# Kernel tuning notes

Measured on AMD Instinct MI355X. Metric: run time of the kernel, lower is better.

Reference implementation:

```python
import jax, jax.numpy as jnp
import numpy as np

NEG_SLOPE = 0.2  # PyG GATConv default


def gat_layer(x, W, att_src, att_dst, bias, src, dst, concat):
    # x: [N, F_in]; W: [F_in, H*C]; att_src/att_dst: [H, C]; bias: [H*C] or [C]
    N = x.shape[0]
    H, C = att_src.shape
    h = (x @ W).reshape(N, H, C)                       # [N, H, C]
    a_s = jnp.einsum('nhc,hc->nh', h, att_src)         # [N, H]
    a_d = jnp.einsum('nhc,hc->nh', h, att_dst)
    e = jax.nn.leaky_relu(a_s[src] + a_d[dst], NEG_SLOPE)  # [E, H]
    # segment softmax over incoming edges of each destination node
    m = jax.ops.segment_max(e, dst, num_segments=N)
    m = jnp.where(jnp.isfinite(m), m, 0.0)
    ee = jnp.exp(e - m[dst])
    s = jax.ops.segment_sum(ee, dst, num_segments=N)
    alpha = ee / (s[dst] + 1e-16)                      # [E, H]
    out = jax.ops.segment_sum(h[src] * alpha[:, :, None], dst, num_segments=N)  # [N, H, C]
    out = out.reshape(N, H * C) if concat else out.mean(axis=1)
    return out + bias


def setup_inputs() -> dict:
    key = jax.random.key(0)
    ks = jax.random.split(key, 16)
    N, E, F_IN, NC = 100000, 3200000, 256, 40
    H, C = 8, 8  # hidden GATConv: heads=8, out=8 -> width 64
    inp = {}
    inp['features'] = jax.random.normal(ks[0], (N, F_IN), dtype=jnp.float32)
    inp['edge_index'] = jax.random.randint(ks[1], (2, E), 0, N, dtype=jnp.int64)
    def p(k, shape):
        return jax.random.normal(k, shape, dtype=jnp.float32) * 0.1
    # layer 0: in 256 -> 8 heads x 8 (concat -> 64)
    inp['W0'] = p(ks[2], (F_IN, H * C)); inp['as0'] = p(ks[3], (H, C)); inp['ad0'] = p(ks[4], (H, C)); inp['b0'] = jnp.zeros((H * C,), jnp.float32)
    # layer 1: 64 -> 8 heads x 8 (concat -> 64)
    inp['W1'] = p(ks[5], (H * C, H * C)); inp['as1'] = p(ks[6], (H, C)); inp['ad1'] = p(ks[7], (H, C)); inp['b1'] = jnp.zeros((H * C,), jnp.float32)
    # layer 2: 64 -> 1 head x n_classes (mean/no-concat)
    inp['W2'] = p(ks[8], (H * C, NC)); inp['as2'] = p(ks[9], (1, NC)); inp['ad2'] = p(ks[10], (1, NC)); inp['b2'] = jnp.zeros((NC,), jnp.float32)
    return inp


def reference(features, edge_index, W0, as0, ad0, b0, W1, as1, ad1, b1, W2, as2, ad2, b2):
    N = features.shape[0]
    loops = jnp.arange(N, dtype=edge_index.dtype)  # PyG GATConv adds self-loops by default
    src = jnp.concatenate([edge_index[0], loops])
    dst = jnp.concatenate([edge_index[1], loops])
    x = gat_layer(features, W0, as0, ad0, b0, src, dst, True)
    x = gat_layer(x, W1, as1, ad1, b1, src, dst, True)
    x = gat_layer(x, W2, as2, ad2, b2, src, dst, False)
    return jax.nn.log_softmax(x, axis=-1)
```

## Files before the change

kernel.cpp:

```cpp
#include <hip/hip_runtime.h>
#include <hip/hip_bf16.h>

#define NEG_SLOPE 0.2f
#define LOG2E 1.44269504f
#define EPB 8192
#define MAXBUCK 400
#define CAP 9216

typedef __attribute__((ext_vector_type(8))) short short8;
typedef __attribute__((ext_vector_type(4))) float f32x4;

__device__ __forceinline__ unsigned short f2bf(float x) {
    unsigned u = __float_as_uint(x);
    unsigned r = (u + 0x7FFFu + ((u >> 16) & 1u)) >> 16;
    return (unsigned short)r;
}

__device__ __forceinline__ float fexp2(float x) {
    return __builtin_amdgcn_exp2f(x);
}


__global__ __launch_bounds__(256) void binit_k(int* __restrict__ bcurE,
                                               int nbuck) {
    int b = blockIdx.x * 256 + threadIdx.x;
    if (b < nbuck) bcurE[b] = b * CAP;
}

__global__ __launch_bounds__(512) void bscatter_k(
    const int* __restrict__ srcs, const int* __restrict__ dsts,
    int* __restrict__ bcurE, int* __restrict__ pairs, int E, int nbuck) {
    __shared__ int lh[MAXBUCK];
    __shared__ int lbase[MAXBUCK];
    int t = threadIdx.x;
    if (t < nbuck) lh[t] = 0;
    __syncthreads();
    int base = blockIdx.x * EPB;
    int cnt = E - base;
    if (cnt > EPB) cnt = EPB;
    int nq = cnt >> 2;
    const int4* d4p = (const int4*)(dsts + base);
    const int4* s4p = (const int4*)(srcs + base);
    for (int i = t; i < nq; i += 512) {
        int4 d = d4p[i];
        atomicAdd(&lh[d.x >> 8], 1);
        atomicAdd(&lh[d.y >> 8], 1);
        atomicAdd(&lh[d.z >> 8], 1);
        atomicAdd(&lh[d.w >> 8], 1);
    }
    for (int i = (nq << 2) + t; i < cnt; i += 512)
        atomicAdd(&lh[dsts[base + i] >> 8], 1);
    __syncthreads();
    if (t < nbuck) {
        int c = lh[t];
        lbase[t] = c ? atomicAdd(&bcurE[t], c) : 0;
        lh[t] = 0;
    }
    __syncthreads();
    for (int i = t; i < nq; i += 512) {
        int4 d = d4p[i];
        int4 s = s4p[i];
        int b0 = d.x >> 8, b1 = d.y >> 8, b2 = d.z >> 8, b3 = d.w >> 8;
        int r0 = atomicAdd(&lh[b0], 1);
        int r1 = atomicAdd(&lh[b1], 1);
        int r2 = atomicAdd(&lh[b2], 1);
        int r3 = atomicAdd(&lh[b3], 1);
        pairs[lbase[b0] + r0] = (s.x << 8) | (d.x & 255);
        pairs[lbase[b1] + r1] = (s.y << 8) | (d.y & 255);
        pairs[lbase[b2] + r2] = (s.z << 8) | (d.z & 255);
        pairs[lbase[b3] + r3] = (s.w << 8) | (d.w & 255);
    }
    for (int i = (nq << 2) + t; i < cnt; i += 512) {
        int s = srcs[base + i], d = dsts[base + i];
        int r = atomicAdd(&lh[d >> 8], 1);
        pairs[lbase[d >> 8] + r] = (s << 8) | (d & 255);
    }
}

__global__ __launch_bounds__(512) void bscan_k(
    const int* __restrict__ bcurE, int* __restrict__ bstart, int nbuck) {
    __shared__ int csum[512];
    int t = threadIdx.x;
    int v = (t < nbuck) ? bcurE[t] - t * CAP : 0;
    csum[t] = v;
    __syncthreads();
    for (int off = 1; off < 512; off <<= 1) {
        int x = (t >= off) ? csum[t - off] : 0;
        __syncthreads();
        csum[t] += x;
        __syncthreads();
    }
    if (t < nbuck) bstart[t] = csum[t] - v;
}

__global__ __launch_bounds__(512) void bucket_sort_k(
    const int* __restrict__ pairs, const int* __restrict__ bcurE,
    const int* __restrict__ bstart, int* __restrict__ row_ptr,
    int* __restrict__ csr_src, int N, int Etot) {
    __shared__ int lh[256];
    __shared__ int sc[256];
    int b = blockIdx.x;
    int n0 = b << 8;
    int t = threadIdx.x;
    if (t < 256) lh[t] = 0;
    __syncthreads();
    int e0c = b * CAP, e1c = bcurE[b];
    for (int e = e0c + t; e < e1c; e += 512)
        atomicAdd(&lh[pairs[e] & 255], 1);
    __syncthreads();
    if (t < 256) sc[t] = lh[t];
    __syncthreads();
    for (int off = 1; off < 256; off <<= 1) {
        int x = (t < 256 && t >= off) ? sc[t - off] : 0;
        __syncthreads();
        if (t < 256) sc[t] += x;
        __syncthreads();
    }
    int e0g = bstart[b];
    if (t < 256) {
        int cntv = lh[t];
        int excl = sc[t] - cntv;
        int n = n0 + t;
        int rp = e0g + n0 + t + excl;
        if (n < N) {
            row_ptr[n] = rp;
            csr_src[rp] = n << 7;
        }
        lh[t] = rp + 1;
    }
    __syncthreads();
    for (int e = e0c + t; e < e1c; e += 512) {
        int p = pairs[e];
        int pos = atomicAdd(&lh[p & 255], 1);
        csr_src[pos] = (p >> 8) << 7;
    }
    if (b == 0 && t == 0) row_ptr[N] = Etot;
}


template <int K>
__global__ __launch_bounds__(256) void gemm_pack8_k(
    const float* __restrict__ x, const float* __restrict__ W,
    const float* __restrict__ a_src, const float* __restrict__ a_dst,
    char* __restrict__ hrec, float* __restrict__ asb,
    float* __restrict__ adb, int N) {
    constexpr int NT = 4;
    constexpr int KT = K / 32;
    constexpr size_t WF_BYTES = (size_t)KT * NT * 64 * 8 * sizeof(short);
    constexpr size_t H_BYTES = (size_t)64 * 65 * sizeof(float);
    __shared__ alignas(16) char smem[WF_BYTES > H_BYTES ? WF_BYTES : H_BYTES];
    short* Wf = (short*)smem;
    float* hL = (float*)smem;
    int tid = threadIdx.x;
    for (int f = tid; f < KT * NT * 64; f += 256) {
        int lane = f & 63;
        int ntk = f >> 6;
        int nt = ntk % NT, kt = ntk / NT;
        int q = lane >> 4, c = lane & 15;
        int n = nt * 16 + c;
        int k0 = kt * 32 + q * 8;
        short8 frag;
        #pragma unroll
        for (int j = 0; j < 8; ++j)
            frag[j] = (short)f2bf(W[(size_t)(k0 + j) * 64 + n]);
        *(short8*)&Wf[f * 8] = frag;
    }
    __syncthreads();
    int wave = tid >> 6, lane = tid & 63;
    int q = lane >> 4, c = lane & 15;
    int m0 = blockIdx.x * 64 + wave * 16;
    int arow = m0 + c;
    int arl = arow < N ? arow : N - 1;
    f32x4 acc[NT] = {};
    for (int kt = 0; kt < KT; ++kt) {
        const float* xp = x + (size_t)arl * K + kt * 32 + q * 8;
        float4 a0 = *(const float4*)xp;
        float4 a1 = *(const float4*)(xp + 4);
        float av[8] = {a0.x, a0.y, a0.z, a0.w, a1.x, a1.y, a1.z, a1.w};
        short8 af;
        #pragma unroll
        for (int j = 0; j < 8; ++j) af[j] = (short)f2bf(av[j]);
        #pragma unroll
        for (int nt = 0; nt < NT; ++nt) {
            short8 bf = *(const short8*)&Wf[((kt * NT + nt) * 64 + lane) * 8];
            acc[nt] = __builtin_amdgcn_mfma_f32_16x16x32_bf16(af, bf, acc[nt],
                                                              0, 0, 0);
        }
    }
    __syncthreads();
    int lrow = wave * 16 + q * 4;
    #pragma unroll
    for (int nt = 0; nt < NT; ++nt)
        #pragma unroll
        for (int reg = 0; reg < 4; ++reg)
            hL[(lrow + reg) * 65 + nt * 16 + c] = acc[nt][reg];
    __syncthreads();
    #pragma unroll
    for (int it = 0; it < 2; ++it) {
        int id = it * 256 + tid;
        int ln = id >> 3, hd = id & 7;
        int gn = blockIdx.x * 64 + ln;
        if (gn >= N) continue;
        const float* hp = &hL[ln * 65 + hd * 8];
        float as = 0.f, ad = 0.f;
        float hv[8];
        #pragma unroll
        for (int j = 0; j < 8; ++j) {
            hv[j] = hp[j];
            as += hv[j] * a_src[hd * 8 + j];
            ad += hv[j] * a_dst[hd * 8 + j];
        }
        adb[gn * 8 + hd] = ad * LOG2E;
        asb[gn * 8 + hd] = as * LOG2E;
        unsigned short u[8];
        #pragma unroll
        for (int j = 0; j < 8; ++j) u[j] = f2bf(hv[j]);
        uint4 pk;
        pk.x = (unsigned)u[0] | ((unsigned)u[1] << 16);
        pk.y = (unsigned)u[2] | ((unsigned)u[3] << 16);
        pk.z = (unsigned)u[4] | ((unsigned)u[5] << 16);
        pk.w = (unsigned)u[6] | ((unsigned)u[7] << 16);
        *(uint4*)(hrec + (size_t)gn * 128 + hd * 16) = pk;
    }
}


__global__ __launch_bounds__(256) void gemm_pack40_k(
    const float* __restrict__ x, const float* __restrict__ W,
    const float* __restrict__ a_src, const float* __restrict__ a_dst,
    char* __restrict__ rec40, float* __restrict__ adb, int N) {
    constexpr int K = 64, NT = 3, KT = 2;
    constexpr size_t WF_BYTES = (size_t)KT * NT * 64 * 8 * sizeof(short);
    constexpr size_t H_BYTES = (size_t)64 * 41 * sizeof(float);
    __shared__ alignas(16) char smem[WF_BYTES > H_BYTES ? WF_BYTES : H_BYTES];
    short* Wf = (short*)smem;
    float* hL = (float*)smem;
    int tid = threadIdx.x;
    for (int f = tid; f < KT * NT * 64; f += 256) {
        int lane = f & 63;
        int ntk = f >> 6;
        int nt = ntk % NT, kt = ntk / NT;
        int q = lane >> 4, c = lane & 15;
        int n = nt * 16 + c;
        int k0 = kt * 32 + q * 8;
        short8 frag;
        #pragma unroll
        for (int j = 0; j < 8; ++j) {
            float v = (n < 40) ? W[(size_t)(k0 + j) * 40 + n] : 0.f;
            frag[j] = (short)f2bf(v);
        }
        *(short8*)&Wf[f * 8] = frag;
    }
    __syncthreads();
    int wave = tid >> 6, lane = tid & 63;
    int q = lane >> 4, c = lane & 15;
    int m0 = blockIdx.x * 64 + wave * 16;
    int arow = m0 + c;
    int arl = arow < N ? arow : N - 1;
    f32x4 acc[NT] = {};
    for (int kt = 0; kt < KT; ++kt) {
        const float* xp = x + (size_t)arl * K + kt * 32 + q * 8;
        float4 a0 = *(const float4*)xp;
        float4 a1 = *(const float4*)(xp + 4);
        float av[8] = {a0.x, a0.y, a0.z, a0.w, a1.x, a1.y, a1.z, a1.w};
        short8 af;
        #pragma unroll
        for (int j = 0; j < 8; ++j) af[j] = (short)f2bf(av[j]);
        #pragma unroll
        for (int nt = 0; nt < NT; ++nt) {
            short8 bf = *(const short8*)&Wf[((kt * NT + nt) * 64 + lane) * 8];
            acc[nt] = __builtin_amdgcn_mfma_f32_16x16x32_bf16(af, bf, acc[nt],
                                                              0, 0, 0);
        }
    }
    __syncthreads();
    int lrow = wave * 16 + q * 4;
    #pragma unroll
    for (int nt = 0; nt < NT; ++nt) {
        int n = nt * 16 + c;
        if (n >= 40) continue;
        #pragma unroll
        for (int reg = 0; reg < 4; ++reg)
            hL[(lrow + reg) * 41 + n] = acc[nt][reg];
    }
    __syncthreads();
    int ln = tid >> 2, sub = tid & 3;
    int gn = blockIdx.x * 64 + ln;
    float pas = 0.f, pad = 0.f;
    if (gn < N) {
        for (int j = sub; j < 40; j += 4) {
            float hv = hL[ln * 41 + j];
            pas += hv * a_src[j];
            pad += hv * a_dst[j];
        }
    }
    pas += __shfl_xor(pas, 1); pas += __shfl_xor(pas, 2);
    pad += __shfl_xor(pad, 1); pad += __shfl_xor(pad, 2);
    if (gn < N && sub == 0) {
        *(float*)(rec40 + (size_t)gn * 128 + 80) = pas * LOG2E;
        adb[gn] = pad * LOG2E;
    }
    for (int i = tid; i < 64 * 40; i += 256) {
        int n2 = i / 40, ch = i % 40;
        int g2 = blockIdx.x * 64 + n2;
        if (g2 < N)
            *(unsigned short*)(rec40 + (size_t)g2 * 128 + ch * 2) =
                f2bf(hL[n2 * 41 + ch]);
    }
}


#define G64(SUF, JB)                                                          \
    int sv##SUF = __builtin_amdgcn_ds_bpermute((JB) * 4 + g4, sv);            \
    float w##SUF = wb[(JB) + wofs];                                           \
    uint4 hv##SUF =                                                           \
        *(const uint4*)(gbase + (size_t)(unsigned)sv##SUF + hoff);

#define FMA8(SUF, LS)                                                         \
    LS;                                                                       \
    acc0 = fmaf(w##SUF, __uint_as_float(hv##SUF.x << 16), acc0);              \
    acc1 = fmaf(w##SUF, __uint_as_float(hv##SUF.x & 0xFFFF0000u), acc1);      \
    acc2 = fmaf(w##SUF, __uint_as_float(hv##SUF.y << 16), acc2);              \
    acc3 = fmaf(w##SUF, __uint_as_float(hv##SUF.y & 0xFFFF0000u), acc3);      \
    acc4 = fmaf(w##SUF, __uint_as_float(hv##SUF.z << 16), acc4);              \
    acc5 = fmaf(w##SUF, __uint_as_float(hv##SUF.z & 0xFFFF0000u), acc5);      \
    acc6 = fmaf(w##SUF, __uint_as_float(hv##SUF.w << 16), acc6);              \
    acc7 = fmaf(w##SUF, __uint_as_float(hv##SUF.w & 0xFFFF0000u), acc7);

__global__ __launch_bounds__(256) void aggr64_k(
    const char* __restrict__ hrec, const float* __restrict__ asb,
    const float* __restrict__ adb, const int* __restrict__ row_ptr,
    const int* __restrict__ csr_src, const float* __restrict__ bias,
    float* __restrict__ out, int N) {
    __shared__ float wlds[4 * 544];
    int wave = threadIdx.x >> 6;
    int node = blockIdx.x * 4 + wave;
    if (node >= N) return;
    int lane = threadIdx.x & 63;
    const char* gbase = hrec;
    float* wb = wlds + wave * 544;
    int g4 = (lane >> 3) * 4;
    int hoff = (lane & 7) * 16;
    int wofs = (lane & 7) * 68 + (lane >> 3);
    int beg = row_ptr[node], end = row_ptr[node + 1];
    float4 adv0 = *(const float4*)(adb + (size_t)node * 8);
    float4 adv1 = *(const float4*)(adb + (size_t)node * 8 + 4);
    float acc0 = 0.f, acc1 = 0.f, acc2 = 0.f, acc3 = 0.f;
    float acc4 = 0.f, acc5 = 0.f, acc6 = 0.f, acc7 = 0.f;
    float lpart = 0.f;
    for (int i0 = beg; i0 < end; i0 += 64) {
        int tail = end - i0;
        int sv = csr_src[i0 + (lane < tail ? lane : 0)];
        int cnt = tail < 64 ? tail : 64;
        {
            const float* asp =
                (const float*)((const char*)asb + (((unsigned)sv) >> 2));
            float4 s0 = *(const float4*)asp;
            float4 s1 = *(const float4*)(asp + 4);
            float w0 = s0.x + adv0.x; w0 = fmaxf(w0, NEG_SLOPE * w0); w0 = fexp2(w0);
            float w1 = s0.y + adv0.y; w1 = fmaxf(w1, NEG_SLOPE * w1); w1 = fexp2(w1);
            float w2 = s0.z + adv0.z; w2 = fmaxf(w2, NEG_SLOPE * w2); w2 = fexp2(w2);
            float w3 = s0.w + adv0.w; w3 = fmaxf(w3, NEG_SLOPE * w3); w3 = fexp2(w3);
            float w4 = s1.x + adv1.x; w4 = fmaxf(w4, NEG_SLOPE * w4); w4 = fexp2(w4);
            float w5 = s1.y + adv1.y; w5 = fmaxf(w5, NEG_SLOPE * w5); w5 = fexp2(w5);
            float w6 = s1.z + adv1.z; w6 = fmaxf(w6, NEG_SLOPE * w6); w6 = fexp2(w6);
            float w7 = s1.w + adv1.w; w7 = fmaxf(w7, NEG_SLOPE * w7); w7 = fexp2(w7);
            if (lane >= cnt) {
                w0 = 0.f; w1 = 0.f; w2 = 0.f; w3 = 0.f;
                w4 = 0.f; w5 = 0.f; w6 = 0.f; w7 = 0.f;
            }
            wb[lane]          = w0;
            wb[68 + lane]     = w1;
            wb[2 * 68 + lane] = w2;
            wb[3 * 68 + lane] = w3;
            wb[4 * 68 + lane] = w4;
            wb[5 * 68 + lane] = w5;
            wb[6 * 68 + lane] = w6;
            wb[7 * 68 + lane] = w7;
        }
        int j = 0;
        for (; j + 32 <= cnt; j += 32) {
            G64(A, j) G64(B, j + 8) G64(C, j + 16) G64(D, j + 24)
            FMA8(A, lpart += wA) FMA8(B, lpart += wB)
            FMA8(C, lpart += wC) FMA8(D, lpart += wD)
        }
        for (; j < cnt; j += 8) {
            G64(A, j)
            FMA8(A, lpart += wA)
        }
    }
    #pragma unroll
    for (int m = 8; m <= 32; m <<= 1) {
        acc0 += __shfl_xor(acc0, m);
        acc1 += __shfl_xor(acc1, m);
        acc2 += __shfl_xor(acc2, m);
        acc3 += __shfl_xor(acc3, m);
        acc4 += __shfl_xor(acc4, m);
        acc5 += __shfl_xor(acc5, m);
        acc6 += __shfl_xor(acc6, m);
        acc7 += __shfl_xor(acc7, m);
        lpart += __shfl_xor(lpart, m);
    }
    if (lane < 8) {
        float denom = lpart + 1e-16f;
        const float4 b0 = *(const float4*)(bias + lane * 8);
        const float4 b1 = *(const float4*)(bias + lane * 8 + 4);
        float4 o0, o1;
        o0.x = acc0 / denom + b0.x;
        o0.y = acc1 / denom + b0.y;
        o0.z = acc2 / denom + b0.z;
        o0.w = acc3 / denom + b0.w;
        o1.x = acc4 / denom + b1.x;
        o1.y = acc5 / denom + b1.y;
        o1.z = acc6 / denom + b1.z;
        o1.w = acc7 / denom + b1.w;
        float* op = out + (size_t)node * 64 + lane * 8;
        *(float4*)op = o0;
        *(float4*)(op + 4) = o1;
    }
}


#define G40(SUF, JB)                                                          \
    int sv##SUF = __builtin_amdgcn_ds_bpermute((JB) * 4 + g4, sv);            \
    float w##SUF = wb[(JB) + gof];                                            \
    uint4 hv##SUF =                                                           \
        *(const uint4*)(gbase + (size_t)(unsigned)sv##SUF + hoff);

__global__ __launch_bounds__(256) void aggr40_k(
    const char* __restrict__ rec40, const float* __restrict__ adb,
    const int* __restrict__ row_ptr, const int* __restrict__ csr_src,
    const float* __restrict__ bias, float* __restrict__ out, int N) {
    __shared__ float wlds[4 * 104];
    int wave = threadIdx.x >> 6;
    int node = blockIdx.x * 4 + wave;
    if (node >= N) return;
    int lane = threadIdx.x & 63;
    const char* gbase = rec40;
    float* wb = wlds + wave * 104;
    float* epi = wb + 64;
    int g4 = (lane >> 3) * 4;
    int sub = lane & 7;
    int hoff = (sub < 5 ? sub : 0) * 16;
    int gof = lane >> 3;
    int beg = row_ptr[node], end = row_ptr[node + 1];
    float ad = adb[node];
    float acc0 = 0.f, acc1 = 0.f, acc2 = 0.f, acc3 = 0.f;
    float acc4 = 0.f, acc5 = 0.f, acc6 = 0.f, acc7 = 0.f;
    float lpart = 0.f;
    for (int i0 = beg; i0 < end; i0 += 64) {
        int tail = end - i0;
        int sv = csr_src[i0 + (lane < tail ? lane : 0)];
        int cnt = tail < 64 ? tail : 64;
        float as = *(const float*)(rec40 + (size_t)(unsigned)sv + 80);
        float v = as + ad;
        v = fmaxf(v, NEG_SLOPE * v);
        float wv = fexp2(v);
        wv = (lane < cnt) ? wv : 0.f;
        lpart += wv;
        wb[lane] = wv;
        int j = 0;
        for (; j + 32 <= cnt; j += 32) {
            G40(A, j) G40(B, j + 8) G40(C, j + 16) G40(D, j + 24)
            FMA8(A, ) FMA8(B, ) FMA8(C, ) FMA8(D, )
        }
        for (; j < cnt; j += 8) {
            G40(A, j)
            FMA8(A, )
        }
    }
    #pragma unroll
    for (int m = 8; m <= 32; m <<= 1) {
        acc0 += __shfl_xor(acc0, m);
        acc1 += __shfl_xor(acc1, m);
        acc2 += __shfl_xor(acc2, m);
        acc3 += __shfl_xor(acc3, m);
        acc4 += __shfl_xor(acc4, m);
        acc5 += __shfl_xor(acc5, m);
        acc6 += __shfl_xor(acc6, m);
        acc7 += __shfl_xor(acc7, m);
    }
    #pragma unroll
    for (int off = 32; off > 0; off >>= 1) lpart += __shfl_xor(lpart, off);
    float l = lpart;
    if (lane < 5) {
        *(float4*)&epi[lane * 8] = make_float4(acc0, acc1, acc2, acc3);
        *(float4*)&epi[lane * 8 + 4] = make_float4(acc4, acc5, acc6, acc7);
    }
    float accv = (lane < 40) ? epi[lane] : 0.f;
    float val = accv / (l + 1e-16f) + ((lane < 40) ? bias[lane] : 0.f);
    float mval = (lane < 40) ? val : -1e30f;
    #pragma unroll
    for (int off = 32; off > 0; off >>= 1)
        mval = fmaxf(mval, __shfl_xor(mval, off));
    float ex = (lane < 40) ? __expf(val - mval) : 0.f;
    #pragma unroll
    for (int off = 32; off > 0; off >>= 1) ex += __shfl_xor(ex, off);
    if (lane < 40)
        out[(size_t)node * 40 + lane] = val - mval - __logf(ex);
}


extern "C" void kernel_launch(void* const* d_in, const int* in_sizes, int n_in,
                              void* d_out, int out_size, void* d_ws,
                              size_t ws_size, hipStream_t stream) {
    const float* features = (const float*)d_in[0];
    const int* edge_index = (const int*)d_in[1];
    const float* W0 = (const float*)d_in[2];
    const float* as0 = (const float*)d_in[3];
    const float* ad0 = (const float*)d_in[4];
    const float* b0 = (const float*)d_in[5];
    const float* W1 = (const float*)d_in[6];
    const float* as1 = (const float*)d_in[7];
    const float* ad1 = (const float*)d_in[8];
    const float* b1 = (const float*)d_in[9];
    const float* W2 = (const float*)d_in[10];
    const float* as2 = (const float*)d_in[11];
    const float* ad2 = (const float*)d_in[12];
    const float* b2 = (const float*)d_in[13];

    int N = in_sizes[0] / 256;
    int E = in_sizes[1] / 2;
    int Etot = E + N;
    int nbuck = (N + 255) >> 8;
    const int* srcs = edge_index;
    const int* dsts = edge_index + E;

    float* ws = (float*)d_ws;
    float* Hbuf = ws;
    float* Abuf = Hbuf + (size_t)N * 64;
    float* adb  = Abuf + (size_t)N * 64;
    float* asb  = adb + (size_t)N * 8;
    char* hrec  = (char*)(asb + (size_t)N * 8);
    int* row_ptr = (int*)(hrec + (size_t)N * 128);
    int* bcurE   = row_ptr + (N + 2);
    int* bstart  = bcurE + MAXBUCK;
    int* csr_src = bstart + MAXBUCK;
    int* pairs   = (int*)Hbuf;

    const int B = 256;
    int gAg = (N + 3) / 4;
    int gGm = (N + 63) / 64;
    int gSc = (E + EPB - 1) / EPB;
    int gBi = (nbuck + 255) / 256;

    binit_k<<<gBi, B, 0, stream>>>(bcurE, nbuck);
    bscatter_k<<<gSc, 512, 0, stream>>>(srcs, dsts, bcurE, pairs, E, nbuck);
    bscan_k<<<1, 512, 0, stream>>>(bcurE, bstart, nbuck);
    bucket_sort_k<<<nbuck, 512, 0, stream>>>(pairs, bcurE, bstart, row_ptr,
                                             csr_src, N, Etot);

    gemm_pack8_k<256><<<gGm, B, 0, stream>>>(features, W0, as0, ad0, hrec,
                                             asb, adb, N);
    aggr64_k<<<gAg, B, 0, stream>>>(hrec, asb, adb, row_ptr, csr_src, b0,
                                    Abuf, N);

    gemm_pack8_k<64><<<gGm, B, 0, stream>>>(Abuf, W1, as1, ad1, hrec, asb,
                                            adb, N);
    aggr64_k<<<gAg, B, 0, stream>>>(hrec, asb, adb, row_ptr, csr_src, b1,
                                    Abuf, N);

    gemm_pack40_k<<<gGm, B, 0, stream>>>(Abuf, W2, as2, ad2, hrec, adb, N);
    aggr40_k<<<gAg, B, 0, stream>>>(hrec, adb, row_ptr, csr_src, b2,
                                    (float*)d_out, N);
}
```

Measured before the change: 525.3 us.

## Fuse layer-0 GEMM with edge bucket scatter and fold bucket scan into sort

Combines the first-layer feature GEMM and the edge bucket-scatter into one launch, interleaving scatter blocks among GEMM blocks so the compute-bound and memory-bound phases overlap. It also drops the bucket-init kernel in favour of a memset with base offsets computed locally, and replaces the separate single-block scan kernel by a redundant per-block scan inside bucket_sort. This cuts several launches and serial gaps. In exchange, scatter now runs with 256 threads instead of 512, shared memory is sized to the largest user, and every sort block repeats the 512-wide scan.

```diff
diff --git a/kernel.cpp b/kernel.cpp
--- a/kernel.cpp
+++ b/kernel.cpp
@@ -21,43 +21,121 @@
 }
 
 
-__global__ __launch_bounds__(256) void binit_k(int* __restrict__ bcurE,
-                                               int nbuck) {
-    int b = blockIdx.x * 256 + threadIdx.x;
-    if (b < nbuck) bcurE[b] = b * CAP;
-}
-
-__global__ __launch_bounds__(512) void bscatter_k(
-    const int* __restrict__ srcs, const int* __restrict__ dsts,
-    int* __restrict__ bcurE, int* __restrict__ pairs, int E, int nbuck) {
-    __shared__ int lh[MAXBUCK];
-    __shared__ int lbase[MAXBUCK];
+template <int K>
+__device__ __forceinline__ void gemm_body(
+    int gb, const float* __restrict__ x, const float* __restrict__ W,
+    const float* __restrict__ a_src, const float* __restrict__ a_dst,
+    char* __restrict__ hrec, float* __restrict__ asb,
+    float* __restrict__ adb, int N, char* smem) {
+    constexpr int NT = 4;
+    constexpr int KT = K / 32;
+    short* Wf = (short*)smem;
+    float* hL = (float*)smem;
+    int tid = threadIdx.x;
+    for (int f = tid; f < KT * NT * 64; f += 256) {
+        int lane = f & 63;
+        int ntk = f >> 6;
+        int nt = ntk % NT, kt = ntk / NT;
+        int q = lane >> 4, c = lane & 15;
+        int n = nt * 16 + c;
+        int k0 = kt * 32 + q * 8;
+        short8 frag;
+        #pragma unroll
+        for (int j = 0; j < 8; ++j)
+            frag[j] = (short)f2bf(W[(size_t)(k0 + j) * 64 + n]);
+        *(short8*)&Wf[f * 8] = frag;
+    }
+    __syncthreads();
+    int wave = tid >> 6, lane = tid & 63;
+    int q = lane >> 4, c = lane & 15;
+    int m0 = gb * 64 + wave * 16;
+    int arow = m0 + c;
+    int arl = arow < N ? arow : N - 1;
+    f32x4 acc[NT] = {};
+    for (int kt = 0; kt < KT; ++kt) {
+        const float* xp = x + (size_t)arl * K + kt * 32 + q * 8;
+        float4 a0 = *(const float4*)xp;
+        float4 a1 = *(const float4*)(xp + 4);
+        float av[8] = {a0.x, a0.y, a0.z, a0.w, a1.x, a1.y, a1.z, a1.w};
+        short8 af;
+        #pragma unroll
+        for (int j = 0; j < 8; ++j) af[j] = (short)f2bf(av[j]);
+        #pragma unroll
+        for (int nt = 0; nt < NT; ++nt) {
+            short8 bf = *(const short8*)&Wf[((kt * NT + nt) * 64 + lane) * 8];
+            acc[nt] = __builtin_amdgcn_mfma_f32_16x16x32_bf16(af, bf, acc[nt],
+                                                              0, 0, 0);
+        }
+    }
+    __syncthreads();
+    int lrow = wave * 16 + q * 4;
+    #pragma unroll
+    for (int nt = 0; nt < NT; ++nt)
+        #pragma unroll
+        for (int reg = 0; reg < 4; ++reg)
+            hL[(lrow + reg) * 65 + nt * 16 + c] = acc[nt][reg];
+    __syncthreads();
+    #pragma unroll
+    for (int it = 0; it < 2; ++it) {
+        int id = it * 256 + tid;
+        int ln = id >> 3, hd = id & 7;
+        int gn = gb * 64 + ln;
+        if (gn >= N) continue;
+        const float* hp = &hL[ln * 65 + hd * 8];
+        float as = 0.f, ad = 0.f;
+        float hv[8];
+        #pragma unroll
+        for (int j = 0; j < 8; ++j) {
+            hv[j] = hp[j];
+            as += hv[j] * a_src[hd * 8 + j];
+            ad += hv[j] * a_dst[hd * 8 + j];
+        }
+        adb[gn * 8 + hd] = ad * LOG2E;
+        asb[gn * 8 + hd] = as * LOG2E;
+        unsigned short u[8];
+        #pragma unroll
+        for (int j = 0; j < 8; ++j) u[j] = f2bf(hv[j]);
+        uint4 pk;
+        pk.x = (unsigned)u[0] | ((unsigned)u[1] << 16);
+        pk.y = (unsigned)u[2] | ((unsigned)u[3] << 16);
+        pk.z = (unsigned)u[4] | ((unsigned)u[5] << 16);
+        pk.w = (unsigned)u[6] | ((unsigned)u[7] << 16);
+        *(uint4*)(hrec + (size_t)gn * 128 + hd * 16) = pk;
+    }
+}
+
+__device__ __forceinline__ void scatter_body(
+    int sb, const int* __restrict__ srcs, const int* __restrict__ dsts,
+    int* __restrict__ bcnt, int* __restrict__ pairs, int E, int nbuck,
+    char* smem) {
+    int* lh = (int*)smem;
+    int* lbase = lh + MAXBUCK;
     int t = threadIdx.x;
-    if (t < nbuck) lh[t] = 0;
-    __syncthreads();
-    int base = blockIdx.x * EPB;
+    for (int i = t; i < nbuck; i += 256) lh[i] = 0;
+    __syncthreads();
+    int base = sb * EPB;
     int cnt = E - base;
     if (cnt > EPB) cnt = EPB;
     int nq = cnt >> 2;
     const int4* d4p = (const int4*)(dsts + base);
     const int4* s4p = (const int4*)(srcs + base);
-    for (int i = t; i < nq; i += 512) {
+    for (int i = t; i < nq; i += 256) {
         int4 d = d4p[i];
         atomicAdd(&lh[d.x >> 8], 1);
         atomicAdd(&lh[d.y >> 8], 1);
         atomicAdd(&lh[d.z >> 8], 1);
         atomicAdd(&lh[d.w >> 8], 1);
     }
-    for (int i = (nq << 2) + t; i < cnt; i += 512)
+    for (int i = (nq << 2) + t; i < cnt; i += 256)
         atomicAdd(&lh[dsts[base + i] >> 8], 1);
     __syncthreads();
-    if (t < nbuck) {
-        int c = lh[t];
-        lbase[t] = c ? atomicAdd(&bcurE[t], c) : 0;
-        lh[t] = 0;
-    }
-    __syncthreads();
-    for (int i = t; i < nq; i += 512) {
+    for (int i = t; i < nbuck; i += 256) {
+        int c = lh[i];
+        lbase[i] = i * CAP + (c ? atomicAdd(&bcnt[i], c) : 0);
+        lh[i] = 0;
+    }
+    __syncthreads();
+    for (int i = t; i < nq; i += 256) {
         int4 d = d4p[i];
         int4 s = s4p[i];
         int b0 = d.x >> 8, b1 = d.y >> 8, b2 = d.z >> 8, b3 = d.w >> 8;
@@ -70,41 +148,69 @@
         pairs[lbase[b2] + r2] = (s.z << 8) | (d.z & 255);
         pairs[lbase[b3] + r3] = (s.w << 8) | (d.w & 255);
     }
-    for (int i = (nq << 2) + t; i < cnt; i += 512) {
+    for (int i = (nq << 2) + t; i < cnt; i += 256) {
         int s = srcs[base + i], d = dsts[base + i];
         int r = atomicAdd(&lh[d >> 8], 1);
         pairs[lbase[d >> 8] + r] = (s << 8) | (d & 255);
     }
 }
 
-__global__ __launch_bounds__(512) void bscan_k(
-    const int* __restrict__ bcurE, int* __restrict__ bstart, int nbuck) {
-    __shared__ int csum[512];
-    int t = threadIdx.x;
-    int v = (t < nbuck) ? bcurE[t] - t * CAP : 0;
-    csum[t] = v;
-    __syncthreads();
-    for (int off = 1; off < 512; off <<= 1) {
-        int x = (t >= off) ? csum[t - off] : 0;
-        __syncthreads();
-        csum[t] += x;
-        __syncthreads();
-    }
-    if (t < nbuck) bstart[t] = csum[t] - v;
+__global__ __launch_bounds__(256) void gemm0_scatter_k(
+    const float* __restrict__ x, const float* __restrict__ W,
+    const float* __restrict__ a_src, const float* __restrict__ a_dst,
+    char* __restrict__ hrec, float* __restrict__ asb,
+    float* __restrict__ adb, int N,
+    const int* __restrict__ srcs, const int* __restrict__ dsts,
+    int* __restrict__ bcnt, int* __restrict__ pairs, int E, int nbuck,
+    int gGm, int gSc, int interleaved) {
+    constexpr size_t WF_BYTES = (size_t)8 * 4 * 64 * 8 * sizeof(short);
+    constexpr size_t H_BYTES = (size_t)64 * 65 * sizeof(float);
+    constexpr size_t SC_BYTES = (size_t)2 * MAXBUCK * sizeof(int);
+    constexpr size_t SM = WF_BYTES > H_BYTES
+                              ? (WF_BYTES > SC_BYTES ? WF_BYTES : SC_BYTES)
+                              : (H_BYTES > SC_BYTES ? H_BYTES : SC_BYTES);
+    __shared__ alignas(16) char smem[SM];
+    int b = blockIdx.x;
+    int isScat, idx;
+    if (interleaved) {
+        isScat = ((b % 5) == 4);
+        idx = isScat ? (b / 5) : (b - (b + 1) / 5);
+    } else {
+        isScat = (b >= gGm);
+        idx = isScat ? (b - gGm) : b;
+    }
+    if (isScat) {
+        if (idx < gSc)
+            scatter_body(idx, srcs, dsts, bcnt, pairs, E, nbuck, smem);
+        return;
+    }
+    gemm_body<256>(idx, x, W, a_src, a_dst, hrec, asb, adb, N, smem);
 }
 
 __global__ __launch_bounds__(512) void bucket_sort_k(
-    const int* __restrict__ pairs, const int* __restrict__ bcurE,
-    const int* __restrict__ bstart, int* __restrict__ row_ptr,
-    int* __restrict__ csr_src, int N, int Etot) {
+    const int* __restrict__ pairs, const int* __restrict__ bcnt,
+    int* __restrict__ row_ptr, int* __restrict__ csr_src, int N, int Etot,
+    int nbuck) {
     __shared__ int lh[256];
     __shared__ int sc[256];
+    __shared__ int bsc[512];
     int b = blockIdx.x;
     int n0 = b << 8;
     int t = threadIdx.x;
+    int v = (t < nbuck) ? bcnt[t] : 0;
+    bsc[t] = v;
+    __syncthreads();
+    for (int off = 1; off < 512; off <<= 1) {
+        int x = (t >= off) ? bsc[t - off] : 0;
+        __syncthreads();
+        bsc[t] += x;
+        __syncthreads();
+    }
+    int e0g = (b > 0) ? bsc[b - 1] : 0;
+    int myCnt = bsc[b] - e0g;
     if (t < 256) lh[t] = 0;
     __syncthreads();
-    int e0c = b * CAP, e1c = bcurE[b];
+    int e0c = b * CAP, e1c = e0c + myCnt;
     for (int e = e0c + t; e < e1c; e += 512)
         atomicAdd(&lh[pairs[e] & 255], 1);
     __syncthreads();
@@ -116,7 +222,6 @@
         if (t < 256) sc[t] += x;
         __syncthreads();
     }
-    int e0g = bstart[b];
     if (t < 256) {
         int cntv = lh[t];
         int excl = sc[t] - cntv;
@@ -138,90 +243,15 @@
 }
 
 
-template <int K>
-__global__ __launch_bounds__(256) void gemm_pack8_k(
+__global__ __launch_bounds__(256) void gemm_pack8_k64(
     const float* __restrict__ x, const float* __restrict__ W,
     const float* __restrict__ a_src, const float* __restrict__ a_dst,
     char* __restrict__ hrec, float* __restrict__ asb,
     float* __restrict__ adb, int N) {
-    constexpr int NT = 4;
-    constexpr int KT = K / 32;
-    constexpr size_t WF_BYTES = (size_t)KT * NT * 64 * 8 * sizeof(short);
+    constexpr size_t WF_BYTES = (size_t)2 * 4 * 64 * 8 * sizeof(short);
     constexpr size_t H_BYTES = (size_t)64 * 65 * sizeof(float);
     __shared__ alignas(16) char smem[WF_BYTES > H_BYTES ? WF_BYTES : H_BYTES];
-    short* Wf = (short*)smem;
-    float* hL = (float*)smem;
-    int tid = threadIdx.x;
-    for (int f = tid; f < KT * NT * 64; f += 256) {
-        int lane = f & 63;
-        int ntk = f >> 6;
-        int nt = ntk % NT, kt = ntk / NT;
-        int q = lane >> 4, c = lane & 15;
-        int n = nt * 16 + c;
-        int k0 = kt * 32 + q * 8;
-        short8 frag;
-        #pragma unroll
-        for (int j = 0; j < 8; ++j)
-            frag[j] = (short)f2bf(W[(size_t)(k0 + j) * 64 + n]);
-        *(short8*)&Wf[f * 8] = frag;
-    }
-    __syncthreads();
-    int wave = tid >> 6, lane = tid & 63;
-    int q = lane >> 4, c = lane & 15;
-    int m0 = blockIdx.x * 64 + wave * 16;
-    int arow = m0 + c;
-    int arl = arow < N ? arow : N - 1;
-    f32x4 acc[NT] = {};
-    for (int kt = 0; kt < KT; ++kt) {
-        const float* xp = x + (size_t)arl * K + kt * 32 + q * 8;
-        float4 a0 = *(const float4*)xp;
-        float4 a1 = *(const float4*)(xp + 4);
-        float av[8] = {a0.x, a0.y, a0.z, a0.w, a1.x, a1.y, a1.z, a1.w};
-        short8 af;
-        #pragma unroll
-        for (int j = 0; j < 8; ++j) af[j] = (short)f2bf(av[j]);
-        #pragma unroll
-        for (int nt = 0; nt < NT; ++nt) {
-            short8 bf = *(const short8*)&Wf[((kt * NT + nt) * 64 + lane) * 8];
-            acc[nt] = __builtin_amdgcn_mfma_f32_16x16x32_bf16(af, bf, acc[nt],
-                                                              0, 0, 0);
-        }
-    }
-    __syncthreads();
-    int lrow = wave * 16 + q * 4;
-    #pragma unroll
-    for (int nt = 0; nt < NT; ++nt)
-        #pragma unroll
-        for (int reg = 0; reg < 4; ++reg)
-            hL[(lrow + reg) * 65 + nt * 16 + c] = acc[nt][reg];
-    __syncthreads();
-    #pragma unroll
-    for (int it = 0; it < 2; ++it) {
-        int id = it * 256 + tid;
-        int ln = id >> 3, hd = id & 7;
-        int gn = blockIdx.x * 64 + ln;
-        if (gn >= N) continue;
-        const float* hp = &hL[ln * 65 + hd * 8];
-        float as = 0.f, ad = 0.f;
-        float hv[8];
-        #pragma unroll
-        for (int j = 0; j < 8; ++j) {
-            hv[j] = hp[j];
-            as += hv[j] * a_src[hd * 8 + j];
-            ad += hv[j] * a_dst[hd * 8 + j];
-        }
-        adb[gn * 8 + hd] = ad * LOG2E;
-        asb[gn * 8 + hd] = as * LOG2E;
-        unsigned short u[8];
-        #pragma unroll
-        for (int j = 0; j < 8; ++j) u[j] = f2bf(hv[j]);
-        uint4 pk;
-        pk.x = (unsigned)u[0] | ((unsigned)u[1] << 16);
-        pk.y = (unsigned)u[2] | ((unsigned)u[3] << 16);
-        pk.z = (unsigned)u[4] | ((unsigned)u[5] << 16);
-        pk.w = (unsigned)u[6] | ((unsigned)u[7] << 16);
-        *(uint4*)(hrec + (size_t)gn * 128 + hd * 16) = pk;
-    }
+    gemm_body<64>(blockIdx.x, x, W, a_src, a_dst, hrec, asb, adb, N, smem);
 }
 
 
@@ -423,8 +453,8 @@
 
 #define G40(SUF, JB)                                                          \
     int sv##SUF = __builtin_amdgcn_ds_bpermute((JB) * 4 + g4, sv);            \
-    float w##SUF = wb[(JB) + gof];                                            \
-    uint4 hv##SUF =                                                           \
+    float w##SUF = wb[(JB) + gof];                                           \
+    uint4 hv##SUF =                                                          \
         *(const uint4*)(gbase + (size_t)(unsigned)sv##SUF + hoff);
 
 __global__ __launch_bounds__(256) void aggr40_k(
@@ -533,30 +563,32 @@
     float* asb  = adb + (size_t)N * 8;
     char* hrec  = (char*)(asb + (size_t)N * 8);
     int* row_ptr = (int*)(hrec + (size_t)N * 128);
-    int* bcurE   = row_ptr + (N + 2);
-    int* bstart  = bcurE + MAXBUCK;
-    int* csr_src = bstart + MAXBUCK;
+    int* bcnt    = row_ptr + (N + 2);
+    int* csr_src = bcnt + MAXBUCK;
     int* pairs   = (int*)Hbuf;
 
     const int B = 256;
     int gAg = (N + 3) / 4;
     int gGm = (N + 63) / 64;
     int gSc = (E + EPB - 1) / EPB;
-    int gBi = (nbuck + 255) / 256;
-
-    binit_k<<<gBi, B, 0, stream>>>(bcurE, nbuck);
-    bscatter_k<<<gSc, 512, 0, stream>>>(srcs, dsts, bcurE, pairs, E, nbuck);
-    bscan_k<<<1, 512, 0, stream>>>(bcurE, bstart, nbuck);
-    bucket_sort_k<<<nbuck, 512, 0, stream>>>(pairs, bcurE, bstart, row_ptr,
-                                             csr_src, N, Etot);
-
-    gemm_pack8_k<256><<<gGm, B, 0, stream>>>(features, W0, as0, ad0, hrec,
-                                             asb, adb, N);
+    int interleaved = (4 * gSc >= gGm) ? 1 : 0;
+    int gFuse = interleaved ? 5 * gSc : gGm + gSc;
+
+    (void)hipMemsetAsync(bcnt, 0, MAXBUCK * 4, stream);
+
+    gemm0_scatter_k<<<gFuse, B, 0, stream>>>(features, W0, as0, ad0, hrec,
+                                             asb, adb, N, srcs, dsts, bcnt,
+                                             pairs, E, nbuck, gGm, gSc,
+                                             interleaved);
+
+    bucket_sort_k<<<nbuck, 512, 0, stream>>>(pairs, bcnt, row_ptr, csr_src,
+                                             N, Etot, nbuck);
+
     aggr64_k<<<gAg, B, 0, stream>>>(hrec, asb, adb, row_ptr, csr_src, b0,
                                     Abuf, N);
 
-    gemm_pack8_k<64><<<gGm, B, 0, stream>>>(Abuf, W1, as1, ad1, hrec, asb,
-                                            adb, N);
+    gemm_pack8_k64<<<gGm, B, 0, stream>>>(Abuf, W1, as1, ad1, hrec, asb,
+                                          adb, N);
     aggr64_k<<<gAg, B, 0, stream>>>(hrec, asb, adb, row_ptr, csr_src, b1,
                                     Abuf, N);
 
```

After: 525.3 us. Within noise of the previous version (+0.0%).
